# Optimization experiments

Measured on AMD Instinct MI355X. Metric: run time of the kernel, lower is better.

The kernel has to match this reference:

```python
import jax, jax.numpy as jnp
import numpy as np

B, N, DIM, FDIM = 1, 4, 128, 128
H = W = 256          # BEV spatial size
FH = FW = 32         # image feature map size
IMG_H = IMG_W = 256
QW1 = QW2 = 16       # query window
FW1 = FW2 = 2        # feature window
HEADS, DH = 4, 32
LN_EPS = 1e-5
BN_EPS = 1e-5


def _gen_grid(h, w):
    xs = jnp.linspace(0.0, 1.0, w)
    ys = jnp.linspace(0.0, 1.0, h)
    gx, gy = jnp.meshgrid(xs, ys, indexing='xy')
    return jnp.stack([gx, gy, jnp.ones_like(gx)], 0)  # (3, h, w)


def _bev_world():
    # BEVEmbedding.grid0 with bev 256x256, 100m x 100m, offset 0, scale 1
    h_m = w_m = 100.0
    Vm = jnp.array([[0.0, -W / w_m, W / 2.0],
                    [-H / h_m, 0.0, H / 2.0],
                    [0.0, 0.0, 1.0]], dtype=jnp.float32)
    g = _gen_grid(H, W)
    g = g.at[0].multiply(W).at[1].multiply(H)
    g = (jnp.linalg.inv(Vm) @ g.reshape(3, -1)).reshape(3, H, W)
    return g[:2]  # (2, H, W)


def _image_plane():
    p = _gen_grid(FH, FW)
    return p.at[0].multiply(IMG_W).at[1].multiply(IMG_H)  # (3, fh, fw)


def _ln(x, g, b):
    m = x.mean(-1, keepdims=True)
    v = ((x - m) ** 2).mean(-1, keepdims=True)
    return (x - m) * jax.lax.rsqrt(v + LN_EPS) * g + b


def _bn_relu_conv(x, g, b, m, v, w):
    # eval-mode BatchNorm2d -> ReLU -> 1x1 conv (no bias); x: (B*, C, h, w)
    xn = (x - m[:, None, None]) * jax.lax.rsqrt(v[:, None, None] + BN_EPS) * g[:, None, None] + b[:, None, None]
    return jnp.einsum('oi,bihw->bohw', w, jax.nn.relu(xn))


def _part_local(t, w1, w2):
    # 'b n d (x w1) (y w2) -> b n x y w1 w2 d'
    b, n, d, h, w = t.shape
    return t.reshape(b, n, d, h // w1, w1, w // w2, w2).transpose(0, 1, 3, 5, 4, 6, 2)


def _part_grid(t, w1, w2):
    b, n, d, h, w = t.shape
    return t.reshape(b, n, d, w1, h // w1, w2, w // w2).transpose(0, 1, 4, 6, 3, 5, 2)


def _merge(z):
    # 'b x y w1 w2 d -> b (x w1) (y w2) d'
    b, x, y, w1, w2, d = z.shape
    return z.transpose(0, 1, 3, 2, 4, 5).reshape(b, x * w1, y * w2, d)


def _win_attend(q, k, v, nq_g, nq_b, nk_g, nk_b, nv_g, nv_b,
                wq, bq, wk, bk, wv, bv, wp, bp, skip):
    # q: (b,n,X,Y,W1,W2,d); k,v: (b,n,X,Y,F1,F2,d) with X*Y windows matching
    b, n, X, Y, W1, W2, d = q.shape
    F1, F2 = k.shape[4], k.shape[5]
    L = X * Y
    q = q.transpose(0, 2, 3, 1, 4, 5, 6).reshape(b, L, n * W1 * W2, d)
    k = k.transpose(0, 2, 3, 1, 4, 5, 6).reshape(b, L, n * F1 * F2, d)
    v = v.transpose(0, 2, 3, 1, 4, 5, 6).reshape(b, L, n * F1 * F2, d)
    q = (_ln(q, nq_g, nq_b) @ wq.T + bq).reshape(b, L, -1, HEADS, DH)
    k = (_ln(k, nk_g, nk_b) @ wk.T + bk).reshape(b, L, -1, HEADS, DH)
    v = (_ln(v, nv_g, nv_b) @ wv.T + bv).reshape(b, L, -1, HEADS, DH)
    dot = (DH ** -0.5) * jnp.einsum('blqmd,blkmd->blmqk', q, k)
    att = jax.nn.softmax(dot, axis=-1)
    a = jnp.einsum('blmqk,blkmd->blqmd', att, v).reshape(b, L, n * W1 * W2, HEADS * DH)
    z = (a @ wp.T + bp).reshape(b, X, Y, n, W1, W2, d).mean(3)  # mean over views
    return z + skip


def _mlp_res(x, g, b, w1, b1, w2, b2):
    h = _ln(x, g, b)
    h = jax.nn.gelu(h @ w1.T + b1, approximate=False) @ w2.T + b2
    return x + h


def _forward(x, feature, I_inv, E_inv,
             fl_bn_g, fl_bn_b, fl_bn_m, fl_bn_v, fl_w,
             fp_bn_g, fp_bn_b, fp_bn_m, fp_bn_v, fp_w,
             bev_w, bev_b, img_w, cam_w,
             a1_nq_g, a1_nq_b, a1_wq, a1_bq, a1_nk_g, a1_nk_b, a1_wk, a1_bk,
             a1_nv_g, a1_nv_b, a1_wv, a1_bv, a1_wp, a1_bp,
             pn1_g, pn1_b, m1_w1, m1_b1, m1_w2, m1_b2,
             a2_nq_g, a2_nq_b, a2_wq, a2_bq, a2_nk_g, a2_nk_b, a2_wk, a2_bk,
             a2_nv_g, a2_nv_b, a2_wv, a2_bv, a2_wp, a2_bp,
             pn2_g, pn2_b, m2_w1, m2_b1, m2_w2, m2_b2,
             post_g, post_b):
    b, n = feature.shape[:2]
    pixel = _image_plane().reshape(3, -1)                       # (3, fh*fw)
    # camera-center embedding: 1x1 conv (no bias) on E_inv last column
    c_embed = jnp.einsum('oi,bni->bno', cam_w, E_inv[..., -1])  # (b,n,dim)
    # ray directions
    cam = jnp.einsum('bnij,jp->bnip', I_inv, pixel)             # (b,n,3,hw)
    cam = jnp.concatenate([cam, jnp.ones_like(cam[:, :, :1])], 2)
    dvec = jnp.einsum('bnij,bnjp->bnip', E_inv, cam)            # (b,n,4,hw)
    img_embed = jnp.einsum('oi,bnip->bnop', img_w, dvec) - c_embed[..., None]
    img_embed = img_embed / (jnp.linalg.norm(img_embed, axis=2, keepdims=True) + 1e-7)
    img_embed = img_embed.reshape(b, n, DIM, FH, FW)
    # BEV positional embedding
    world = _bev_world()                                        # (2,H,W)
    w_embed = jnp.einsum('oi,ihw->ohw', bev_w, world) + bev_b[:, None, None]
    bev_embed = w_embed[None, None] - c_embed[..., None, None]  # (b,n,dim,H,W)
    query_pos = bev_embed / (jnp.linalg.norm(bev_embed, axis=2, keepdims=True) + 1e-7)
    # key/value features
    feat_flat = feature.reshape(b * n, FDIM, FH, FW)
    key = img_embed + _bn_relu_conv(feat_flat, fp_bn_g, fp_bn_b, fp_bn_m, fp_bn_v, fp_w).reshape(b, n, DIM, FH, FW)
    val = _bn_relu_conv(feat_flat, fl_bn_g, fl_bn_b, fl_bn_m, fl_bn_v, fl_w).reshape(b, n, DIM, FH, FW)
    query = query_pos + x[:, None]                              # (b,n,dim,H,W)
    # stage 1: local window cross-attention
    q1 = _part_local(query, QW1, QW2)
    k1 = _part_local(key, FW1, FW2)
    v1 = _part_local(val, FW1, FW2)
    skip1 = _part_local(x[:, None], QW1, QW2)[:, 0]
    z = _merge(_win_attend(q1, k1, v1, a1_nq_g, a1_nq_b, a1_nk_g, a1_nk_b,
                           a1_nv_g, a1_nv_b, a1_wq, a1_bq, a1_wk, a1_bk,
                           a1_wv, a1_bv, a1_wp, a1_bp, skip1))   # (b,H,W,d)
    z = _mlp_res(z, pn1_g, pn1_b, m1_w1, m1_b1, m1_w2, m1_b2)
    # stage 2: local query windows vs grid-shuffled key/value windows
    q2 = z.reshape(b, H // QW1, QW1, W // QW2, QW2, DIM).transpose(0, 1, 3, 2, 4, 5)
    skip2 = q2
    q2 = jnp.broadcast_to(q2[:, None], (b, n) + q2.shape[1:])
    k2 = _part_grid(key, FW1, FW2)
    v2 = _part_grid(val, FW1, FW2)
    z = _merge(_win_attend(q2, k2, v2, a2_nq_g, a2_nq_b, a2_nk_g, a2_nk_b,
                           a2_nv_g, a2_nv_b, a2_wq, a2_bq, a2_wk, a2_bk,
                           a2_wv, a2_bv, a2_wp, a2_bp, skip2))
    z = _mlp_res(z, pn2_g, pn2_b, m2_w1, m2_b1, m2_w2, m2_b2)
    z = _ln(z, post_g, post_b)
    return z.transpose(0, 3, 1, 2)                              # (b, d, H, W)


def setup_inputs() -> dict:
    ks = iter(jax.random.split(jax.random.key(0), 64))
    rn = lambda *s: jax.random.normal(next(ks), s, jnp.float32)
    w = lambda *s: rn(*s) * 0.05
    d = {'index': 0}
    d['x'] = rn(B, DIM, H, W)
    d['feature'] = rn(B, N, FDIM, FH, FW)
    d['I_inv'] = rn(B, N, 3, 3)
    d['E_inv'] = rn(B, N, 4, 4)
    for p in ('fl', 'fp'):
        d[p + '_bn_g'] = jnp.ones((FDIM,)); d[p + '_bn_b'] = jnp.zeros((FDIM,))
        d[p + '_bn_m'] = jnp.zeros((FDIM,)); d[p + '_bn_v'] = jnp.ones((FDIM,))
        d[p + '_w'] = w(DIM, FDIM)
    d['bev_w'] = w(DIM, 2); d['bev_b'] = jnp.zeros((DIM,))
    d['img_w'] = w(DIM, 4); d['cam_w'] = w(DIM, 4)
    for i in ('1', '2'):
        for t in ('q', 'k', 'v'):
            d['a%s_n%s_g' % (i, t)] = jnp.ones((DIM,))
            d['a%s_n%s_b' % (i, t)] = jnp.zeros((DIM,))
            d['a%s_w%s' % (i, t)] = w(HEADS * DH, DIM)
            d['a%s_b%s' % (i, t)] = jnp.zeros((HEADS * DH,))
        d['a%s_wp' % i] = w(DIM, HEADS * DH); d['a%s_bp' % i] = jnp.zeros((DIM,))
        d['pn%s_g' % i] = jnp.ones((DIM,)); d['pn%s_b' % i] = jnp.zeros((DIM,))
        d['m%s_w1' % i] = w(2 * DIM, DIM); d['m%s_b1' % i] = jnp.zeros((2 * DIM,))
        d['m%s_w2' % i] = w(DIM, 2 * DIM); d['m%s_b2' % i] = jnp.zeros((DIM,))
    d['post_g'] = jnp.ones((DIM,)); d['post_b'] = jnp.zeros((DIM,))
    return d


def reference(index, x, feature, I_inv, E_inv,
              fl_bn_g, fl_bn_b, fl_bn_m, fl_bn_v, fl_w,
              fp_bn_g, fp_bn_b, fp_bn_m, fp_bn_v, fp_w,
              bev_w, bev_b, img_w, cam_w,
              a1_nq_g, a1_nq_b, a1_wq, a1_bq, a1_nk_g, a1_nk_b, a1_wk, a1_bk,
              a1_nv_g, a1_nv_b, a1_wv, a1_bv, a1_wp, a1_bp,
              pn1_g, pn1_b, m1_w1, m1_b1, m1_w2, m1_b2,
              a2_nq_g, a2_nq_b, a2_wq, a2_bq, a2_nk_g, a2_nk_b, a2_wk, a2_bk,
              a2_nv_g, a2_nv_b, a2_wv, a2_bv, a2_wp, a2_bp,
              pn2_g, pn2_b, m2_w1, m2_b1, m2_w2, m2_b2,
              post_g, post_b):
    # index is fixed to 0 (selects bev.grid0, computed internally)
    return _forward(x, feature, I_inv, E_inv,
                    fl_bn_g, fl_bn_b, fl_bn_m, fl_bn_v, fl_w,
                    fp_bn_g, fp_bn_b, fp_bn_m, fp_bn_v, fp_w,
                    bev_w, bev_b, img_w, cam_w,
                    a1_nq_g, a1_nq_b, a1_wq, a1_bq, a1_nk_g, a1_nk_b, a1_wk, a1_bk,
                    a1_nv_g, a1_nv_b, a1_wv, a1_bv, a1_wp, a1_bp,
                    pn1_g, pn1_b, m1_w1, m1_b1, m1_w2, m1_b2,
                    a2_nq_g, a2_nq_b, a2_wq, a2_bq, a2_nk_g, a2_nk_b, a2_wk, a2_bk,
                    a2_nv_g, a2_nv_b, a2_wv, a2_bv, a2_wp, a2_bp,
                    pn2_g, pn2_b, m2_w1, m2_b1, m2_w2, m2_b2,
                    post_g, post_b)
```

## Files before the change

### kernel.cpp

```cpp
#include <hip/hip_runtime.h>
#include <math.h>

#define LN_EPS 1e-5f
#define BN_EPS 1e-5f
#define QK_SCALE 0.1767766953f

typedef __attribute__((ext_vector_type(8))) short bf16x8;
typedef __attribute__((ext_vector_type(4))) float f32x4;

__device__ __forceinline__ unsigned short f2bf(float x) {
    union { float f; unsigned u; } v; v.f = x;
    unsigned r = v.u + 0x7FFFu + ((v.u >> 16) & 1u);
    return (unsigned short)(r >> 16);
}
__device__ __forceinline__ float bf2f(unsigned short h) {
    union { unsigned u; float f; } v; v.u = ((unsigned)h) << 16;
    return v.f;
}
__device__ __forceinline__ unsigned packbf(float a, float b) {
    return (unsigned)f2bf(a) | ((unsigned)f2bf(b) << 16);
}
#define FENCE() asm volatile("" ::: "memory")


__global__ void k_pack(unsigned short* __restrict__ dst, float* __restrict__ cb,
    const float* wq1, const float* wp1, const float* wq2, const float* wp2,
    const float* m1w1, const float* m1w2, const float* m2w1, const float* m2w2,
    const float* fpw, const float* flw,
    const float* wk1, const float* wv1, const float* wk2, const float* wv2,
    const float* bev_b, const float* cam_w, const float* E_inv)
{
    int gid = blockIdx.x * 256 + threadIdx.x;
    if (gid < 294912) {
        const float* src; int off = gid;
        if      (off < 16384)  { src = wq1; }
        else if (off < 32768)  { src = wp1;  off -= 16384; }
        else if (off < 49152)  { src = wq2;  off -= 32768; }
        else if (off < 65536)  { src = wp2;  off -= 49152; }
        else if (off < 98304)  { src = m1w1; off -= 65536; }
        else if (off < 131072) { src = m1w2; off -= 98304; }
        else if (off < 163840) { src = m2w1; off -= 131072; }
        else if (off < 196608) { src = m2w2; off -= 163840; }
        else if (off < 212992) { src = fpw;  off -= 196608; }
        else if (off < 229376) { src = flw;  off -= 212992; }
        else if (off < 245760) { src = wk1;  off -= 229376; }
        else if (off < 262144) { src = wv1;  off -= 245760; }
        else if (off < 278528) { src = wk2;  off -= 262144; }
        else                   { src = wv2;  off -= 278528; }
        dst[gid] = f2bf(src[off]);
    } else if (gid < 311296) {
        int off = gid - 294912;
        dst[gid] = f2bf(wq1[(off & 127)*128 + (off >> 7)]);
    } else if (gid < 327680) {
        int off = gid - 311296;
        dst[gid] = f2bf(wq2[(off & 127)*128 + (off >> 7)]);
    } else if (gid < 328192) {
        int i = gid - 327680;
        int n = i >> 7, c = i & 127;
        const float* Ev = E_inv + n * 16;
        cb[i] = bev_b[c] - (cam_w[c*4+0]*Ev[3] + cam_w[c*4+1]*Ev[7]
                          + cam_w[c*4+2]*Ev[11] + cam_w[c*4+3]*Ev[15]);
    }
}

__global__ void k_img_embed(const float* __restrict__ I_inv,
                            const float* __restrict__ E_inv,
                            const float* __restrict__ img_w,
                            const float* __restrict__ cam_w,
                            float* __restrict__ img_embed)
{
    const int blk = blockIdx.x;
    const int n = blk >> 10, p = blk & 1023;
    const int fy = p >> 5, fx = p & 31;
    const float px = fx * (256.0f / 31.0f);
    const float py = fy * (256.0f / 31.0f);
    const float* Iv = I_inv + n * 9;
    const float* Ev = E_inv + n * 16;
    const float c0 = Iv[0]*px + Iv[1]*py + Iv[2];
    const float c1 = Iv[3]*px + Iv[4]*py + Iv[5];
    const float c2 = Iv[6]*px + Iv[7]*py + Iv[8];
    const float d0 = Ev[0]*c0 + Ev[1]*c1 + Ev[2]*c2 + Ev[3];
    const float d1 = Ev[4]*c0 + Ev[5]*c1 + Ev[6]*c2 + Ev[7];
    const float d2 = Ev[8]*c0 + Ev[9]*c1 + Ev[10]*c2 + Ev[11];
    const float d3 = Ev[12]*c0 + Ev[13]*c1 + Ev[14]*c2 + Ev[15];
    const int c = threadIdx.x;
    const float ce = cam_w[c*4+0]*Ev[3] + cam_w[c*4+1]*Ev[7]
                   + cam_w[c*4+2]*Ev[11] + cam_w[c*4+3]*Ev[15];
    float v = img_w[c*4+0]*d0 + img_w[c*4+1]*d1
            + img_w[c*4+2]*d2 + img_w[c*4+3]*d3 - ce;
    __shared__ float red[128];
    red[c] = v * v;
    __syncthreads();
    for (int s = 64; s > 0; s >>= 1) {
        if (c < s) red[c] += red[c + s];
        __syncthreads();
    }
    img_embed[(n*1024 + p)*128 + c] = v / (sqrtf(red[0]) + 1e-7f);
}

__global__ __launch_bounds__(256) void k_keyval(
    const float* __restrict__ feature,
    const float* __restrict__ img_embed,
    const float* __restrict__ fp_g, const float* __restrict__ fp_b,
    const float* __restrict__ fp_m, const float* __restrict__ fp_v,
    const unsigned short* __restrict__ fpw,
    const float* __restrict__ fl_g, const float* __restrict__ fl_b,
    const float* __restrict__ fl_m, const float* __restrict__ fl_v,
    const unsigned short* __restrict__ flw,
    float* __restrict__ key, float* __restrict__ val)
{
    __shared__ __align__(16) unsigned short aP[64*136];
    __shared__ __align__(16) unsigned short aL[64*136];
    const int n = blockIdx.x >> 4, p0 = (blockIdx.x & 15) * 64;
    const int tid = threadIdx.x;

    for (int idx = tid; idx < 8192; idx += 256) {
        int c = idx >> 6, dt = idx & 63;
        float f = feature[(n*128 + c)*1024 + p0 + dt];
        float xp = (f - fp_m[c]) * rsqrtf(fp_v[c] + BN_EPS) * fp_g[c] + fp_b[c];
        float xl = (f - fl_m[c]) * rsqrtf(fl_v[c] + BN_EPS) * fl_g[c] + fl_b[c];
        aP[dt*136 + c] = f2bf(fmaxf(xp, 0.f));
        aL[dt*136 + c] = f2bf(fmaxf(xl, 0.f));
    }
    __syncthreads();

    const int lane = tid & 63, wid = tid >> 6;
    const int lr = lane & 15, lg = lane >> 4;
    const int wtb = wid * 16;
    f32x4 ak[8], av[8];
    const f32x4 z4 = {0.f, 0.f, 0.f, 0.f};
#pragma unroll
    for (int nf = 0; nf < 8; nf++) { ak[nf] = z4; av[nf] = z4; }
#pragma unroll
    for (int kst = 0; kst < 4; kst++) {
        bf16x8 a1 = *(const bf16x8*)&aP[(wtb+lr)*136 + kst*32 + lg*8];
        bf16x8 a2 = *(const bf16x8*)&aL[(wtb+lr)*136 + kst*32 + lg*8];
#pragma unroll
        for (int nf = 0; nf < 8; nf++) {
            bf16x8 bK = *(const bf16x8*)&fpw[(nf*16+lr)*128 + kst*32 + lg*8];
            bf16x8 bV = *(const bf16x8*)&flw[(nf*16+lr)*128 + kst*32 + lg*8];
            ak[nf] = __builtin_amdgcn_mfma_f32_16x16x32_bf16(a1, bK, ak[nf], 0, 0, 0);
            av[nf] = __builtin_amdgcn_mfma_f32_16x16x32_bf16(a2, bV, av[nf], 0, 0, 0);
        }
    }
#pragma unroll
    for (int nf = 0; nf < 8; nf++) {
#pragma unroll
        for (int rr = 0; rr < 4; rr++) {
            int g = (n*1024 + p0 + wtb + lg*4 + rr)*128 + nf*16 + lr;
            key[g] = ak[nf][rr] + img_embed[g];
            val[g] = av[nf][rr];
        }
    }
}

__global__ __launch_bounds__(256) void k_kvproj(
    const float* __restrict__ key, const float* __restrict__ val,
    const float* __restrict__ k1g, const float* __restrict__ k1b,
    const unsigned short* __restrict__ wk1, const float* __restrict__ bk1,
    const float* __restrict__ v1g, const float* __restrict__ v1b,
    const unsigned short* __restrict__ wv1, const float* __restrict__ bv1,
    const float* __restrict__ k2g, const float* __restrict__ k2b,
    const unsigned short* __restrict__ wk2, const float* __restrict__ bk2,
    const float* __restrict__ v2g, const float* __restrict__ v2b,
    const unsigned short* __restrict__ wv2, const float* __restrict__ bv2,
    float* __restrict__ kp1, float* __restrict__ vp1,
    float* __restrict__ kp2, float* __restrict__ vp2)
{
    __shared__ __align__(16) unsigned short tile[64*136];
    const int pj = blockIdx.x >> 6;
    const int tok0 = (blockIdx.x & 63) * 64;
    const int tid = threadIdx.x;
    const int t = tid >> 2, part = tid & 3;

    const float* gsel[4] = {k1g, v1g, k2g, v2g};
    const float* asel[4] = {k1b, v1b, k2b, v2b};
    const unsigned short* wsel[4] = {wk1, wv1, wk2, wv2};
    const float* bsel[4] = {bk1, bv1, bk2, bv2};
    float* osel[4] = {kp1, vp1, kp2, vp2};
    const float* src = (pj & 1) ? val : key;
    const float* g  = gsel[pj];
    const float* ba = asel[pj];

    float rr_[32];
    float s1 = 0.f, s2 = 0.f;
#pragma unroll
    for (int k4 = 0; k4 < 8; k4++) {
        float4 a = *(const float4*)&src[(tok0+t)*128 + part*32 + k4*4];
        rr_[k4*4+0]=a.x; rr_[k4*4+1]=a.y; rr_[k4*4+2]=a.z; rr_[k4*4+3]=a.w;
        s1 += a.x+a.y+a.z+a.w; s2 += a.x*a.x+a.y*a.y+a.z*a.z+a.w*a.w;
    }
    s1 += __shfl_xor(s1, 1); s1 += __shfl_xor(s1, 2);
    s2 += __shfl_xor(s2, 1); s2 += __shfl_xor(s2, 2);
    const float mean = s1*(1.f/128.f);
    const float var  = s2*(1.f/128.f) - mean*mean;
    const float rstd = rsqrtf(var + LN_EPS);
#pragma unroll
    for (int k = 0; k < 32; k++) {
        int c = part*32 + k;
        float hat = (rr_[k]-mean)*rstd;
        tile[t*136 + c] = f2bf(hat*g[c] + ba[c]);
    }
    FENCE();

    const int lane = tid & 63, wid = tid >> 6;
    const int lr = lane & 15, lg = lane >> 4;
    const int wtb = wid * 16;
    const unsigned short* wp_ = wsel[pj];
    const f32x4 z4 = {0.f, 0.f, 0.f, 0.f};
    f32x4 acc[8];
#pragma unroll
    for (int nf = 0; nf < 8; nf++) acc[nf] = z4;
#pragma unroll
    for (int kst = 0; kst < 4; kst++) {
        bf16x8 a = *(const bf16x8*)&tile[(wtb+lr)*136 + kst*32 + lg*8];
#pragma unroll
        for (int nf = 0; nf < 8; nf++) {
            bf16x8 b = *(const bf16x8*)&wp_[(nf*16+lr)*128 + kst*32 + lg*8];
            acc[nf] = __builtin_amdgcn_mfma_f32_16x16x32_bf16(a, b, acc[nf], 0, 0, 0);
        }
    }
    float* outp = osel[pj];
#pragma unroll
    for (int nf = 0; nf < 8; nf++) {
        float bb = bsel[pj][nf*16 + lr];
#pragma unroll
        for (int rr2 = 0; rr2 < 4; rr2++)
            outp[(tok0 + wtb + lg*4 + rr2)*128 + nf*16 + lr] = acc[nf][rr2] + bb;
    }
}

__global__ __launch_bounds__(256) void k_mwin(
    const float* __restrict__ kp1, const float* __restrict__ kp2,
    const unsigned short* __restrict__ wq1T, const unsigned short* __restrict__ wq2T,
    const float* __restrict__ bq1, const float* __restrict__ bq2,
    unsigned short* __restrict__ Mw1, unsigned short* __restrict__ Mw2,
    float* __restrict__ Mb1, float* __restrict__ Mb2)
{
    __shared__ __align__(16) unsigned short kt[16*136];
    const int blk = blockIdx.x;
    const int stage = blk >> 8, win = blk & 255;
    const int wx = win >> 4, wy = win & 15;
    const int tid = threadIdx.x;

    const float* kp = stage ? kp2 : kp1;
    const unsigned short* wqT = stage ? wq2T : wq1T;
    const float* bq = stage ? bq2 : bq1;
    unsigned short* Mw = stage ? Mw2 : Mw1;
    float* Mb = stage ? Mb2 : Mb1;

    for (int idx = tid; idx < 2048; idx += 256) {
        int c = idx & 127, j = idx >> 7;
        int nk = j >> 2, f1 = (j >> 1) & 1, f2 = j & 1;
        int tok = stage ? (nk*1024 + (f1*16+wx)*32 + (f2*16+wy))
                        : (nk*1024 + (wx*2+f1)*32 + (wy*2+f2));
        kt[j*136 + c] = f2bf(kp[tok*128 + c]);
    }
    __syncthreads();

    const int lane = tid & 63, wid = tid >> 6;
    const int lr = lane & 15, lg = lane >> 4;
    const f32x4 z4 = {0.f, 0.f, 0.f, 0.f};
#pragma unroll
    for (int cc = 0; cc < 2; cc++) {
        int ct = wid*2 + cc;
#pragma unroll
        for (int hd = 0; hd < 4; hd++) {
            bf16x8 a = *(const bf16x8*)&kt[lr*136 + hd*32 + lg*8];
            bf16x8 b = *(const bf16x8*)&wqT[(ct*16+lr)*128 + hd*32 + lg*8];
            f32x4 acc = __builtin_amdgcn_mfma_f32_16x16x32_bf16(a, b, z4, 0, 0, 0);
#pragma unroll
            for (int rr = 0; rr < 4; rr++)
                Mw[((win*4 + hd)*16 + lg*4 + rr)*128 + ct*16 + lr]
                    = f2bf(acc[rr] * QK_SCALE);
        }
    }
    if (tid < 64) {
        int hd = tid >> 4, ky = tid & 15;
        float s = 0.f;
        for (int d = 0; d < 32; d++)
            s += bq[hd*32 + d] * bf2f(kt[ky*136 + hd*32 + d]);
        Mb[win*64 + tid] = s * QK_SCALE;
    }
}

__global__ __launch_bounds__(256) void k_attn1(
    const float* __restrict__ x,
    const float* __restrict__ vp,
    const unsigned short* __restrict__ mw, const float* __restrict__ mb,
    const float* __restrict__ bev_w, const float* __restrict__ cb,
    const float* __restrict__ nqg, const float* __restrict__ nqb,
    const unsigned short* __restrict__ wpp, const float* __restrict__ bp,
    float* __restrict__ z1)
{
    __shared__ __align__(16) unsigned short aT[64*136];
    __shared__ __align__(16) unsigned short mws[64*136];
    __shared__ __align__(16) unsigned short vbT[128*24];
    __shared__ __align__(16) unsigned short xbuf[64*132];
    __shared__ float mbs[64];
    __shared__ float cbs[512];
    __shared__ float nqgs[128];
    __shared__ float nqbs[128];

    const int blk = blockIdx.x;
    const int win = blk >> 2, rg = blk & 3;
    const int wx = win >> 4, wy = win & 15;
    const int tid = threadIdx.x;
    const int lane = tid & 63, wid = tid >> 6;
    const int lr = lane & 15, lg = lane >> 4;
    const int wtb = wid * 16;

    for (int idx = tid; idx < 2048; idx += 256) {
        int c = idx & 127, j = idx >> 7;
        int nk = j >> 2, f1 = (j >> 1) & 1, f2 = j & 1;
        int src = (nk*1024 + (wx*2+f1)*32 + (wy*2+f2))*128 + c;
        vbT[c*24 + j] = f2bf(vp[src]);
    }
    {
        const unsigned short* mwsrc = mw + win*8192;
        for (int idx = tid; idx < 2048; idx += 256) {
            int row = idx >> 5, c4 = (idx & 31)*4;
            *(ushort4*)&mws[row*136 + c4] = *(const ushort4*)&mwsrc[row*128 + c4];
        }
    }
    for (int idx = tid; idx < 8192; idx += 256) {
        int tt = idx & 63, c = idx >> 6;
        int hh = wx*16 + rg*4 + (tt >> 4), ww = wy*16 + (tt & 15);
        xbuf[tt*132 + c] = f2bf(x[c*65536 + hh*256 + ww]);
    }
    if (tid < 64) mbs[tid] = mb[win*64 + tid];
    for (int idx = tid; idx < 512; idx += 256) cbs[idx] = cb[idx];
    if (tid < 128) { nqgs[tid] = nqg[tid]; nqbs[tid] = nqb[tid]; }

    const int t = tid >> 2, part = tid & 3;
    const int w1 = rg*4 + (t >> 4), w2 = t & 15;
    const int h = wx*16 + w1, w = wy*16 + w2;
    const float world0 = 50.f - (float)h * (100.f/255.f);
    const float world1 = 50.f - (float)w * (100.f/255.f);

    float xv[32];
#pragma unroll
    for (int k = 0; k < 32; k++) xv[k] = x[(part*32+k)*65536 + h*256 + w];
    float base_[32];
#pragma unroll
    for (int k = 0; k < 32; k++) {
        int c = part*32 + k;
        base_[k] = bev_w[c*2+0]*world0 + bev_w[c*2+1]*world1;
    }
    __syncthreads();

    f32x4 aacc[4][2];
    const f32x4 z4 = {0.f, 0.f, 0.f, 0.f};
#pragma unroll
    for (int hd = 0; hd < 4; hd++) { aacc[hd][0] = z4; aacc[hd][1] = z4; }

    uint2 pa[4], pb[4];

    auto do_view = [&](int n, uint2* pp) {
        float r[32]; float ss = 0.f;
#pragma unroll
        for (int k = 0; k < 32; k++) {
            int c = part*32 + k;
            float e = base_[k] + cbs[n*128 + c];
            r[k] = e; ss += e*e;
        }
        ss += __shfl_xor(ss, 1); ss += __shfl_xor(ss, 2);
        const float invn = 1.f / (sqrtf(ss) + 1e-7f);
        float s1 = 0.f, s2 = 0.f;
#pragma unroll
        for (int k = 0; k < 32; k++) {
            float qv = r[k]*invn + xv[k];
            r[k] = qv; s1 += qv; s2 += qv*qv;
        }
        s1 += __shfl_xor(s1, 1); s1 += __shfl_xor(s1, 2);
        s2 += __shfl_xor(s2, 1); s2 += __shfl_xor(s2, 2);
        const float mean = s1*(1.f/128.f);
        const float var  = s2*(1.f/128.f) - mean*mean;
        const float rstd = rsqrtf(var + LN_EPS);
#pragma unroll
        for (int k4 = 0; k4 < 8; k4++) {
            int c = part*32 + k4*4;
            ushort4 u;
            u.x = f2bf((r[k4*4+0]-mean)*rstd*nqgs[c+0] + nqbs[c+0]);
            u.y = f2bf((r[k4*4+1]-mean)*rstd*nqgs[c+1] + nqbs[c+1]);
            u.z = f2bf((r[k4*4+2]-mean)*rstd*nqgs[c+2] + nqbs[c+2]);
            u.w = f2bf((r[k4*4+3]-mean)*rstd*nqgs[c+3] + nqbs[c+3]);
            *(ushort4*)&aT[t*136 + c] = u;
        }
        FENCE();

        f32x4 sacc[4];
#pragma unroll
        for (int hd = 0; hd < 4; hd++) sacc[hd] = z4;
#pragma unroll
        for (int kst = 0; kst < 4; kst++) {
            bf16x8 bq_ = *(const bf16x8*)&aT[(wtb+lr)*136 + kst*32 + lg*8];
#pragma unroll
            for (int hd = 0; hd < 4; hd++) {
                bf16x8 am = *(const bf16x8*)&mws[(hd*16 + lr)*136 + kst*32 + lg*8];
                sacc[hd] = __builtin_amdgcn_mfma_f32_16x16x32_bf16(am, bq_, sacc[hd], 0, 0, 0);
            }
        }
#pragma unroll
        for (int hd = 0; hd < 4; hd++) {
            float e0 = sacc[hd][0] + mbs[hd*16 + lg*4 + 0];
            float e1 = sacc[hd][1] + mbs[hd*16 + lg*4 + 1];
            float e2 = sacc[hd][2] + mbs[hd*16 + lg*4 + 2];
            float e3 = sacc[hd][3] + mbs[hd*16 + lg*4 + 3];
            float mx = fmaxf(fmaxf(e0, e1), fmaxf(e2, e3));
            mx = fmaxf(mx, __shfl_xor(mx, 16));
            mx = fmaxf(mx, __shfl_xor(mx, 32));
            e0 = __expf(e0-mx); e1 = __expf(e1-mx);
            e2 = __expf(e2-mx); e3 = __expf(e3-mx);
            float sum = e0+e1+e2+e3;
            sum += __shfl_xor(sum, 16);
            sum += __shfl_xor(sum, 32);
            float is = 1.f/sum;
            pp[hd] = make_uint2(packbf(e0*is, e1*is), packbf(e2*is, e3*is));
        }
        FENCE();
    };

    auto pv_pair = [&]() {
        const int s0 = (lg & 1)*32 + lr;
        const int s1 = s0 + 16;
        const bool hi = (lg >> 1) != 0;
#pragma unroll
        for (int hd = 0; hd < 4; hd++) {
            unsigned a00 = __shfl(pa[hd].x, s0), a01 = __shfl(pa[hd].y, s0);
            unsigned a10 = __shfl(pa[hd].x, s1), a11 = __shfl(pa[hd].y, s1);
            unsigned b00 = __shfl(pb[hd].x, s0), b01 = __shfl(pb[hd].y, s0);
            unsigned b10 = __shfl(pb[hd].x, s1), b11 = __shfl(pb[hd].y, s1);
            union { unsigned u[4]; bf16x8 v; } af;
            af.u[0] = hi ? b00 : a00; af.u[1] = hi ? b01 : a01;
            af.u[2] = hi ? b10 : a10; af.u[3] = hi ? b11 : a11;
#pragma unroll
            for (int dt = 0; dt < 2; dt++) {
                bf16x8 bv = *(const bf16x8*)&vbT[(hd*32+dt*16+lr)*24 + (lg&1)*8];
                aacc[hd][dt] = __builtin_amdgcn_mfma_f32_16x16x32_bf16(af.v, bv, aacc[hd][dt], 0, 0, 0);
            }
        }
    };

    do_view(0, pa); do_view(1, pb); pv_pair();
    do_view(2, pa); do_view(3, pb); pv_pair();

#pragma unroll
    for (int hd = 0; hd < 4; hd++)
#pragma unroll
        for (int dt = 0; dt < 2; dt++)
#pragma unroll
            for (int rr = 0; rr < 4; rr++)
                aT[(wtb + lg*4 + rr)*136 + hd*32 + dt*16 + lr]
                    = f2bf(aacc[hd][dt][rr] * 0.25f);
    FENCE();

    f32x4 acc[8];
#pragma unroll
    for (int nf = 0; nf < 8; nf++) acc[nf] = z4;
#pragma unroll
    for (int kst = 0; kst < 4; kst++) {
        bf16x8 a = *(const bf16x8*)&aT[(wtb+lr)*136 + kst*32 + lg*8];
#pragma unroll
        for (int nf = 0; nf < 8; nf++) {
            bf16x8 b = *(const bf16x8*)&wpp[(nf*16+lr)*128 + kst*32 + lg*8];
            acc[nf] = __builtin_amdgcn_mfma_f32_16x16x32_bf16(a, b, acc[nf], 0, 0, 0);
        }
    }
#pragma unroll
    for (int nf = 0; nf < 8; nf++) {
        float bpv = bp[nf*16 + lr];
#pragma unroll
        for (int rr = 0; rr < 4; rr++) {
            int tt = wtb + lg*4 + rr;
            int hh = wx*16 + rg*4 + (tt >> 4), ww = wy*16 + (tt & 15);
            float res = bf2f(xbuf[tt*132 + nf*16 + lr]);
            z1[(hh*256+ww)*128 + nf*16 + lr] = acc[nf][rr] + bpv + res;
        }
    }
}

__global__ __launch_bounds__(256) void k_attn2(
    const float* __restrict__ z1,
    const float* __restrict__ vp,
    const unsigned short* __restrict__ mw, const float* __restrict__ mb,
    const float* __restrict__ nqg, const float* __restrict__ nqb,
    const unsigned short* __restrict__ wpp, const float* __restrict__ bp,
    float* __restrict__ z2)
{
    __shared__ __align__(16) unsigned short aT[64*136];
    __shared__ __align__(16) unsigned short vbT[128*24];
    __shared__ float mbs[64];

    const int blk = blockIdx.x;
    const int win = blk >> 2, rg = blk & 3;
    const int wx = win >> 4, wy = win & 15;
    const int tid = threadIdx.x;
    const int lane = tid & 63, wid = tid >> 6;
    const int lr = lane & 15, lg = lane >> 4;
    const int wtb = wid * 16;

    for (int idx = tid; idx < 2048; idx += 256) {
        int c = idx & 127, j = idx >> 7;
        int nk = j >> 2, f1 = (j >> 1) & 1, f2 = j & 1;
        int src = (nk*1024 + (f1*16+wx)*32 + (f2*16+wy))*128 + c;
        vbT[c*24 + j] = f2bf(vp[src]);
    }
    if (tid < 64) mbs[tid] = mb[win*64 + tid];

    const int t = tid >> 2, part = tid & 3;
    const int w1 = rg*4 + (t >> 4), w2 = t & 15;
    const int h = wx*16 + w1, w = wy*16 + w2;
    const float* zr = z1 + (h*256 + w)*128 + part*32;

    float r[32]; float s1 = 0.f, s2 = 0.f;
#pragma unroll
    for (int k4 = 0; k4 < 8; k4++) {
        float4 v = *(const float4*)&zr[k4*4];
        r[k4*4+0]=v.x; r[k4*4+1]=v.y; r[k4*4+2]=v.z; r[k4*4+3]=v.w;
        s1 += v.x+v.y+v.z+v.w;
        s2 += v.x*v.x+v.y*v.y+v.z*v.z+v.w*v.w;
    }
    s1 += __shfl_xor(s1, 1); s1 += __shfl_xor(s1, 2);
    s2 += __shfl_xor(s2, 1); s2 += __shfl_xor(s2, 2);
    const float mean = s1*(1.f/128.f);
    const float var  = s2*(1.f/128.f) - mean*mean;
    const float rstd = rsqrtf(var + LN_EPS);
#pragma unroll
    for (int k4 = 0; k4 < 8; k4++) {
        int c = part*32 + k4*4;
        ushort4 u;
        u.x = f2bf((r[k4*4+0]-mean)*rstd*nqg[c+0] + nqb[c+0]);
        u.y = f2bf((r[k4*4+1]-mean)*rstd*nqg[c+1] + nqb[c+1]);
        u.z = f2bf((r[k4*4+2]-mean)*rstd*nqg[c+2] + nqb[c+2]);
        u.w = f2bf((r[k4*4+3]-mean)*rstd*nqg[c+3] + nqb[c+3]);
        *(ushort4*)&aT[t*136 + c] = u;
    }
    __syncthreads();

    const f32x4 z4 = {0.f, 0.f, 0.f, 0.f};
    f32x4 sacc[4];
#pragma unroll
    for (int hd = 0; hd < 4; hd++) sacc[hd] = z4;
#pragma unroll
    for (int kst = 0; kst < 4; kst++) {
        bf16x8 bq_ = *(const bf16x8*)&aT[(wtb+lr)*136 + kst*32 + lg*8];
#pragma unroll
        for (int hd = 0; hd < 4; hd++) {
            bf16x8 am = *(const bf16x8*)&mw[((win*4+hd)*16 + lr)*128 + kst*32 + lg*8];
            sacc[hd] = __builtin_amdgcn_mfma_f32_16x16x32_bf16(am, bq_, sacc[hd], 0, 0, 0);
        }
    }
    uint2 pa[4];
#pragma unroll
    for (int hd = 0; hd < 4; hd++) {
        float e0 = sacc[hd][0] + mbs[hd*16 + lg*4 + 0];
        float e1 = sacc[hd][1] + mbs[hd*16 + lg*4 + 1];
        float e2 = sacc[hd][2] + mbs[hd*16 + lg*4 + 2];
        float e3 = sacc[hd][3] + mbs[hd*16 + lg*4 + 3];
        float mx = fmaxf(fmaxf(e0, e1), fmaxf(e2, e3));
        mx = fmaxf(mx, __shfl_xor(mx, 16));
        mx = fmaxf(mx, __shfl_xor(mx, 32));
        e0 = __expf(e0-mx); e1 = __expf(e1-mx);
        e2 = __expf(e2-mx); e3 = __expf(e3-mx);
        float sum = e0+e1+e2+e3;
        sum += __shfl_xor(sum, 16);
        sum += __shfl_xor(sum, 32);
        float is = 1.f/sum;
        pa[hd] = make_uint2(packbf(e0*is, e1*is), packbf(e2*is, e3*is));
    }

    f32x4 aacc[4][2];
#pragma unroll
    for (int hd = 0; hd < 4; hd++) { aacc[hd][0] = z4; aacc[hd][1] = z4; }
    {
        const int s0 = (lg & 1)*32 + lr;
        const int s1_ = s0 + 16;
        const bool hi = (lg >> 1) != 0;
#pragma unroll
        for (int hd = 0; hd < 4; hd++) {
            unsigned a00 = __shfl(pa[hd].x, s0), a01 = __shfl(pa[hd].y, s0);
            unsigned a10 = __shfl(pa[hd].x, s1_), a11 = __shfl(pa[hd].y, s1_);
            union { unsigned u[4]; bf16x8 v; } af;
            af.u[0] = hi ? 0u : a00; af.u[1] = hi ? 0u : a01;
            af.u[2] = hi ? 0u : a10; af.u[3] = hi ? 0u : a11;
#pragma unroll
            for (int dt = 0; dt < 2; dt++) {
                bf16x8 bv = *(const bf16x8*)&vbT[(hd*32+dt*16+lr)*24 + (lg&1)*8];
                aacc[hd][dt] = __builtin_amdgcn_mfma_f32_16x16x32_bf16(af.v, bv, aacc[hd][dt], 0, 0, 0);
            }
        }
    }
    FENCE();
#pragma unroll
    for (int hd = 0; hd < 4; hd++)
#pragma unroll
        for (int dt = 0; dt < 2; dt++)
#pragma unroll
            for (int rr = 0; rr < 4; rr++)
                aT[(wtb + lg*4 + rr)*136 + hd*32 + dt*16 + lr]
                    = f2bf(aacc[hd][dt][rr]);
    FENCE();

    f32x4 acc[8];
#pragma unroll
    for (int nf = 0; nf < 8; nf++) acc[nf] = z4;
#pragma unroll
    for (int kst = 0; kst < 4; kst++) {
        bf16x8 a = *(const bf16x8*)&aT[(wtb+lr)*136 + kst*32 + lg*8];
#pragma unroll
        for (int nf = 0; nf < 8; nf++) {
            bf16x8 b = *(const bf16x8*)&wpp[(nf*16+lr)*128 + kst*32 + lg*8];
            acc[nf] = __builtin_amdgcn_mfma_f32_16x16x32_bf16(a, b, acc[nf], 0, 0, 0);
        }
    }
#pragma unroll
    for (int nf = 0; nf < 8; nf++) {
        float bpv = bp[nf*16 + lr];
#pragma unroll
        for (int rr = 0; rr < 4; rr++) {
            int tt = wtb + lg*4 + rr;
            int hh = wx*16 + rg*4 + (tt >> 4), ww = wy*16 + (tt & 15);
            int gi = (hh*256+ww)*128 + nf*16 + lr;
            z2[gi] = acc[nf][rr] + bpv + z1[gi];
        }
    }
}

__global__ __launch_bounds__(256) void k_mlp(
    float* __restrict__ z,
    const float* __restrict__ g, const float* __restrict__ bta,
    const unsigned short* __restrict__ w1p, const float* __restrict__ b1,
    const unsigned short* __restrict__ w2p, const float* __restrict__ b2)
{
    __shared__ __align__(16) unsigned short aT[64*136];
    __shared__ __align__(16) unsigned short hT[64*136];
    const int base = blockIdx.x * 64;
    const int tid = threadIdx.x;
    const int t = tid >> 2, part = tid & 3;

    const float* zr = z + (base + t)*128 + part*32;
    float r[32]; float s1 = 0.f, s2 = 0.f;
#pragma unroll
    for (int k4 = 0; k4 < 8; k4++) {
        float4 v = *(const float4*)&zr[k4*4];
        r[k4*4+0]=v.x; r[k4*4+1]=v.y; r[k4*4+2]=v.z; r[k4*4+3]=v.w;
        s1 += v.x+v.y+v.z+v.w;
        s2 += v.x*v.x+v.y*v.y+v.z*v.z+v.w*v.w;
    }
    s1 += __shfl_xor(s1, 1); s1 += __shfl_xor(s1, 2);
    s2 += __shfl_xor(s2, 1); s2 += __shfl_xor(s2, 2);
    const float mean = s1*(1.f/128.f);
    const float var  = s2*(1.f/128.f) - mean*mean;
    const float rstd = rsqrtf(var + LN_EPS);
#pragma unroll
    for (int k4 = 0; k4 < 8; k4++) {
        int c = part*32 + k4*4;
        ushort4 u;
        u.x = f2bf((r[k4*4+0]-mean)*rstd*g[c+0] + bta[c+0]);
        u.y = f2bf((r[k4*4+1]-mean)*rstd*g[c+1] + bta[c+1]);
        u.z = f2bf((r[k4*4+2]-mean)*rstd*g[c+2] + bta[c+2]);
        u.w = f2bf((r[k4*4+3]-mean)*rstd*g[c+3] + bta[c+3]);
        *(ushort4*)&aT[t*136 + c] = u;
    }
    __syncthreads();

    const int lane = tid & 63, wid = tid >> 6;
    const int lr = lane & 15, lg = lane >> 4;
    const int wtb = wid * 16;
    const f32x4 z4 = {0.f, 0.f, 0.f, 0.f};

    f32x4 oacc[8];
#pragma unroll
    for (int nf = 0; nf < 8; nf++) oacc[nf] = z4;

#pragma unroll
    for (int half = 0; half < 2; half++) {
        f32x4 acc[8];
#pragma unroll
        for (int nf = 0; nf < 8; nf++) acc[nf] = z4;
#pragma unroll
        for (int kst = 0; kst < 4; kst++) {
            bf16x8 a = *(const bf16x8*)&aT[(wtb+lr)*136 + kst*32 + lg*8];
#pragma unroll
            for (int nf = 0; nf < 8; nf++) {
                bf16x8 b = *(const bf16x8*)&w1p[((half*8+nf)*16+lr)*128 + kst*32 + lg*8];
                acc[nf] = __builtin_amdgcn_mfma_f32_16x16x32_bf16(a, b, acc[nf], 0, 0, 0);
            }
        }
#pragma unroll
        for (int nf = 0; nf < 8; nf++) {
            float bb = b1[(half*8+nf)*16 + lr];
#pragma unroll
            for (int rr = 0; rr < 4; rr++) {
                float hv = acc[nf][rr] + bb;
                float gl = 0.5f*hv*(1.f + erff(hv*0.70710678118f));
                hT[(wtb + lg*4 + rr)*136 + nf*16 + lr] = f2bf(gl);
            }
        }
        FENCE();

#pragma unroll
        for (int kst = 0; kst < 4; kst++) {
            bf16x8 a = *(const bf16x8*)&hT[(wtb+lr)*136 + kst*32 + lg*8];
#pragma unroll
            for (int nf = 0; nf < 8; nf++) {
                bf16x8 b = *(const bf16x8*)&w2p[(nf*16+lr)*256 + half*128 + kst*32 + lg*8];
                oacc[nf] = __builtin_amdgcn_mfma_f32_16x16x32_bf16(a, b, oacc[nf], 0, 0, 0);
            }
        }
        FENCE();
    }

#pragma unroll
    for (int nf = 0; nf < 8; nf++) {
        float bb = b2[nf*16 + lr];
#pragma unroll
        for (int rr = 0; rr < 4; rr++) {
            int idx = (base + wtb + lg*4 + rr)*128 + nf*16 + lr;
            z[idx] = z[idx] + oacc[nf][rr] + bb;
        }
    }
}

__global__ __launch_bounds__(256) void k_post(
    const float* __restrict__ z2,
    const float* __restrict__ g, const float* __restrict__ b,
    float* __restrict__ out)
{
    __shared__ float buf[64][129];
    const int blk = blockIdx.x;
    const int h = blk >> 2, w0 = (blk & 3)*64;
    const int tid = threadIdx.x;
    const int t = tid >> 2, part = tid & 3;

    const float* zr = z2 + (h*256 + w0 + t)*128 + part*32;
    float r[32]; float s1 = 0.f, s2 = 0.f;
#pragma unroll
    for (int k4 = 0; k4 < 8; k4++) {
        float4 v = *(const float4*)&zr[k4*4];
        r[k4*4+0]=v.x; r[k4*4+1]=v.y; r[k4*4+2]=v.z; r[k4*4+3]=v.w;
        s1 += v.x+v.y+v.z+v.w;
        s2 += v.x*v.x+v.y*v.y+v.z*v.z+v.w*v.w;
    }
    s1 += __shfl_xor(s1, 1); s1 += __shfl_xor(s1, 2);
    s2 += __shfl_xor(s2, 1); s2 += __shfl_xor(s2, 2);
    const float mean = s1*(1.f/128.f);
    const float var  = s2*(1.f/128.f) - mean*mean;
    const float rstd = rsqrtf(var + LN_EPS);
#pragma unroll
    for (int k = 0; k < 32; k++) {
        int c = part*32 + k;
        buf[t][c] = (r[k]-mean)*rstd*g[c] + b[c];
    }
    __syncthreads();
    for (int idx = tid; idx < 64*128; idx += 256) {
        int c = idx >> 6, wl = idx & 63;
        out[(c*256 + h)*256 + w0 + wl] = buf[wl][c];
    }
}

extern "C" void kernel_launch(void* const* d_in, const int* in_sizes, int n_in,
                              void* d_out, int out_size, void* d_ws, size_t ws_size,
                              hipStream_t stream)
{
    (void)in_sizes; (void)n_in; (void)out_size; (void)ws_size;
    const float* x       = (const float*)d_in[1];
    const float* feature = (const float*)d_in[2];
    const float* I_inv   = (const float*)d_in[3];
    const float* E_inv   = (const float*)d_in[4];
    const float* fl_g = (const float*)d_in[5],  *fl_b = (const float*)d_in[6];
    const float* fl_m = (const float*)d_in[7],  *fl_v = (const float*)d_in[8];
    const float* fl_w = (const float*)d_in[9];
    const float* fp_g = (const float*)d_in[10], *fp_b = (const float*)d_in[11];
    const float* fp_m = (const float*)d_in[12], *fp_v = (const float*)d_in[13];
    const float* fp_w = (const float*)d_in[14];
    const float* bev_w = (const float*)d_in[15], *bev_b = (const float*)d_in[16];
    const float* img_w = (const float*)d_in[17], *cam_w = (const float*)d_in[18];
    const float* a1_nq_g = (const float*)d_in[19], *a1_nq_b = (const float*)d_in[20];
    const float* a1_wq = (const float*)d_in[21], *a1_bq = (const float*)d_in[22];
    const float* a1_nk_g = (const float*)d_in[23], *a1_nk_b = (const float*)d_in[24];
    const float* a1_wk = (const float*)d_in[25], *a1_bk = (const float*)d_in[26];
    const float* a1_nv_g = (const float*)d_in[27], *a1_nv_b = (const float*)d_in[28];
    const float* a1_wv = (const float*)d_in[29], *a1_bv = (const float*)d_in[30];
    const float* a1_wp = (const float*)d_in[31], *a1_bp = (const float*)d_in[32];
    const float* pn1_g = (const float*)d_in[33], *pn1_b = (const float*)d_in[34];
    const float* m1_w1 = (const float*)d_in[35], *m1_b1 = (const float*)d_in[36];
    const float* m1_w2 = (const float*)d_in[37], *m1_b2 = (const float*)d_in[38];
    const float* a2_nq_g = (const float*)d_in[39], *a2_nq_b = (const float*)d_in[40];
    const float* a2_wq = (const float*)d_in[41], *a2_bq = (const float*)d_in[42];
    const float* a2_nk_g = (const float*)d_in[43], *a2_nk_b = (const float*)d_in[44];
    const float* a2_wk = (const float*)d_in[45], *a2_bk = (const float*)d_in[46];
    const float* a2_nv_g = (const float*)d_in[47], *a2_nv_b = (const float*)d_in[48];
    const float* a2_wv = (const float*)d_in[49], *a2_bv = (const float*)d_in[50];
    const float* a2_wp = (const float*)d_in[51], *a2_bp = (const float*)d_in[52];
    const float* pn2_g = (const float*)d_in[53], *pn2_b = (const float*)d_in[54];
    const float* m2_w1 = (const float*)d_in[55], *m2_b1 = (const float*)d_in[56];
    const float* m2_w2 = (const float*)d_in[57], *m2_b2 = (const float*)d_in[58];
    const float* post_g = (const float*)d_in[59], *post_b = (const float*)d_in[60];

    float* ws  = (float*)d_ws;
    unsigned short* pk = (unsigned short*)ws;
    const unsigned short* wp1p  = pk + 16384;
    const unsigned short* wp2p  = pk + 49152;
    const unsigned short* m1w1p = pk + 65536;
    const unsigned short* m1w2p = pk + 98304;
    const unsigned short* m2w1p = pk + 131072;
    const unsigned short* m2w2p = pk + 163840;
    const unsigned short* fpwp  = pk + 196608;
    const unsigned short* flwp  = pk + 212992;
    const unsigned short* wk1p  = pk + 229376;
    const unsigned short* wv1p  = pk + 245760;
    const unsigned short* wk2p  = pk + 262144;
    const unsigned short* wv2p  = pk + 278528;
    const unsigned short* wq1Tp = pk + 294912;
    const unsigned short* wq2Tp = pk + 311296;

    float* cb  = ws + 163840;
    float* Mb1 = ws + 164352;
    float* Mb2 = ws + 180736;
    float* kp2 = ws + 197120;
    float* vp2 = ws + 721408;
    unsigned short* Mw2 = (unsigned short*)(ws + 1245696);
    float* kp1 = ws + 2294272;
    float* vp1 = ws + 2818560;
    unsigned short* Mw1 = (unsigned short*)(ws + 3342848);
    float* key = ws + 3342848;
    float* val = ws + 3867136;
    float* img = ws + 4391424;
    float* z2  = ws + 2294272;
    float* z1  = (float*)d_out;

    k_pack<<<1283, 256, 0, stream>>>(pk, cb,
        a1_wq, a1_wp, a2_wq, a2_wp, m1_w1, m1_w2, m2_w1, m2_w2,
        fp_w, fl_w, a1_wk, a1_wv, a2_wk, a2_wv, bev_b, cam_w, E_inv);
    k_img_embed<<<4096, 128, 0, stream>>>(I_inv, E_inv, img_w, cam_w, img);
    k_keyval<<<64, 256, 0, stream>>>(feature, img,
                                     fp_g, fp_b, fp_m, fp_v, fpwp,
                                     fl_g, fl_b, fl_m, fl_v, flwp,
                                     key, val);
    k_kvproj<<<256, 256, 0, stream>>>(key, val,
                                      a1_nk_g, a1_nk_b, wk1p, a1_bk,
                                      a1_nv_g, a1_nv_b, wv1p, a1_bv,
                                      a2_nk_g, a2_nk_b, wk2p, a2_bk,
                                      a2_nv_g, a2_nv_b, wv2p, a2_bv,
                                      kp1, vp1, kp2, vp2);
    k_mwin<<<512, 256, 0, stream>>>(kp1, kp2, wq1Tp, wq2Tp, a1_bq, a2_bq,
                                    Mw1, Mw2, Mb1, Mb2);
    k_attn1<<<1024, 256, 0, stream>>>(x, vp1, Mw1, Mb1, bev_w, cb,
                                      a1_nq_g, a1_nq_b, wp1p, a1_bp, z1);
    k_mlp<<<1024, 256, 0, stream>>>(z1, pn1_g, pn1_b, m1w1p, m1_b1, m1w2p, m1_b2);
    k_attn2<<<1024, 256, 0, stream>>>(z1, vp2, Mw2, Mb2,
                                      a2_nq_g, a2_nq_b, wp2p, a2_bp, z2);
    k_mlp<<<1024, 256, 0, stream>>>(z2, pn2_g, pn2_b, m2w1p, m2_b1, m2w2p, m2_b2);
    k_post<<<1024, 256, 0, stream>>>(z2, post_g, post_b, (float*)d_out);
}
```

Before: 391.5 us.

## Process 128 rows per MLP block to reuse weight fragments across two row tiles

The MLP kernel now handles 128 tokens per block instead of 64, so each wave computes two 16-row tiles and every weight fragment loaded from global memory feeds two MFMAs. The hidden dimension is processed in four 64-wide chunks, which shrinks the shared hidden buffer, and the grid is halved. The aim is to halve weight load traffic per token. The cost is more accumulator registers, fewer blocks to fill the CUs, and a larger shared-memory footprint.

```diff
diff --git a/kernel.cpp b/kernel.cpp
--- a/kernel.cpp
+++ b/kernel.cpp
@@ -633,35 +633,38 @@
     const unsigned short* __restrict__ w1p, const float* __restrict__ b1,
     const unsigned short* __restrict__ w2p, const float* __restrict__ b2)
 {
-    __shared__ __align__(16) unsigned short aT[64*136];
-    __shared__ __align__(16) unsigned short hT[64*136];
-    const int base = blockIdx.x * 64;
+    __shared__ __align__(16) unsigned short aT[128*136];
+    __shared__ __align__(16) unsigned short hT[128*72];
+    const int base = blockIdx.x * 128;
     const int tid = threadIdx.x;
     const int t = tid >> 2, part = tid & 3;
 
-    const float* zr = z + (base + t)*128 + part*32;
-    float r[32]; float s1 = 0.f, s2 = 0.f;
-#pragma unroll
-    for (int k4 = 0; k4 < 8; k4++) {
-        float4 v = *(const float4*)&zr[k4*4];
-        r[k4*4+0]=v.x; r[k4*4+1]=v.y; r[k4*4+2]=v.z; r[k4*4+3]=v.w;
-        s1 += v.x+v.y+v.z+v.w;
-        s2 += v.x*v.x+v.y*v.y+v.z*v.z+v.w*v.w;
-    }
-    s1 += __shfl_xor(s1, 1); s1 += __shfl_xor(s1, 2);
-    s2 += __shfl_xor(s2, 1); s2 += __shfl_xor(s2, 2);
-    const float mean = s1*(1.f/128.f);
-    const float var  = s2*(1.f/128.f) - mean*mean;
-    const float rstd = rsqrtf(var + LN_EPS);
-#pragma unroll
-    for (int k4 = 0; k4 < 8; k4++) {
-        int c = part*32 + k4*4;
-        ushort4 u;
-        u.x = f2bf((r[k4*4+0]-mean)*rstd*g[c+0] + bta[c+0]);
-        u.y = f2bf((r[k4*4+1]-mean)*rstd*g[c+1] + bta[c+1]);
-        u.z = f2bf((r[k4*4+2]-mean)*rstd*g[c+2] + bta[c+2]);
-        u.w = f2bf((r[k4*4+3]-mean)*rstd*g[c+3] + bta[c+3]);
-        *(ushort4*)&aT[t*136 + c] = u;
+#pragma unroll
+    for (int rt = 0; rt < 2; rt++) {
+        const float* zr = z + (base + rt*64 + t)*128 + part*32;
+        float r[32]; float s1 = 0.f, s2 = 0.f;
+#pragma unroll
+        for (int k4 = 0; k4 < 8; k4++) {
+            float4 v = *(const float4*)&zr[k4*4];
+            r[k4*4+0]=v.x; r[k4*4+1]=v.y; r[k4*4+2]=v.z; r[k4*4+3]=v.w;
+            s1 += v.x+v.y+v.z+v.w;
+            s2 += v.x*v.x+v.y*v.y+v.z*v.z+v.w*v.w;
+        }
+        s1 += __shfl_xor(s1, 1); s1 += __shfl_xor(s1, 2);
+        s2 += __shfl_xor(s2, 1); s2 += __shfl_xor(s2, 2);
+        const float mean = s1*(1.f/128.f);
+        const float var  = s2*(1.f/128.f) - mean*mean;
+        const float rstd = rsqrtf(var + LN_EPS);
+#pragma unroll
+        for (int k4 = 0; k4 < 8; k4++) {
+            int c = part*32 + k4*4;
+            ushort4 u;
+            u.x = f2bf((r[k4*4+0]-mean)*rstd*g[c+0] + bta[c+0]);
+            u.y = f2bf((r[k4*4+1]-mean)*rstd*g[c+1] + bta[c+1]);
+            u.z = f2bf((r[k4*4+2]-mean)*rstd*g[c+2] + bta[c+2]);
+            u.w = f2bf((r[k4*4+3]-mean)*rstd*g[c+3] + bta[c+3]);
+            *(ushort4*)&aT[(rt*64 + t)*136 + c] = u;
+        }
     }
     __syncthreads();
 
@@ -670,43 +673,53 @@
     const int wtb = wid * 16;
     const f32x4 z4 = {0.f, 0.f, 0.f, 0.f};
 
-    f32x4 oacc[8];
-#pragma unroll
-    for (int nf = 0; nf < 8; nf++) oacc[nf] = z4;
-
-#pragma unroll
-    for (int half = 0; half < 2; half++) {
-        f32x4 acc[8];
-#pragma unroll
-        for (int nf = 0; nf < 8; nf++) acc[nf] = z4;
+    f32x4 oacc[2][8];
+#pragma unroll
+    for (int rt = 0; rt < 2; rt++)
+#pragma unroll
+        for (int nf = 0; nf < 8; nf++) oacc[rt][nf] = z4;
+
+#pragma unroll
+    for (int q = 0; q < 4; q++) {
+        f32x4 acc[2][4];
+#pragma unroll
+        for (int rt = 0; rt < 2; rt++)
+#pragma unroll
+            for (int nf = 0; nf < 4; nf++) acc[rt][nf] = z4;
 #pragma unroll
         for (int kst = 0; kst < 4; kst++) {
-            bf16x8 a = *(const bf16x8*)&aT[(wtb+lr)*136 + kst*32 + lg*8];
+            bf16x8 a0 = *(const bf16x8*)&aT[(wtb+lr)*136 + kst*32 + lg*8];
+            bf16x8 a1 = *(const bf16x8*)&aT[(64+wtb+lr)*136 + kst*32 + lg*8];
+#pragma unroll
+            for (int nf = 0; nf < 4; nf++) {
+                bf16x8 b = *(const bf16x8*)&w1p[((q*4+nf)*16+lr)*128 + kst*32 + lg*8];
+                acc[0][nf] = __builtin_amdgcn_mfma_f32_16x16x32_bf16(a0, b, acc[0][nf], 0, 0, 0);
+                acc[1][nf] = __builtin_amdgcn_mfma_f32_16x16x32_bf16(a1, b, acc[1][nf], 0, 0, 0);
+            }
+        }
+#pragma unroll
+        for (int nf = 0; nf < 4; nf++) {
+            float bb = b1[(q*4+nf)*16 + lr];
+#pragma unroll
+            for (int rt = 0; rt < 2; rt++)
+#pragma unroll
+                for (int rr = 0; rr < 4; rr++) {
+                    float hv = acc[rt][nf][rr] + bb;
+                    float gl = 0.5f*hv*(1.f + erff(hv*0.70710678118f));
+                    hT[(rt*64 + wtb + lg*4 + rr)*72 + nf*16 + lr] = f2bf(gl);
+                }
+        }
+        FENCE();
+
+#pragma unroll
+        for (int kst2 = 0; kst2 < 2; kst2++) {
+            bf16x8 a0 = *(const bf16x8*)&hT[(wtb+lr)*72 + kst2*32 + lg*8];
+            bf16x8 a1 = *(const bf16x8*)&hT[(64+wtb+lr)*72 + kst2*32 + lg*8];
 #pragma unroll
             for (int nf = 0; nf < 8; nf++) {
-                bf16x8 b = *(const bf16x8*)&w1p[((half*8+nf)*16+lr)*128 + kst*32 + lg*8];
-                acc[nf] = __builtin_amdgcn_mfma_f32_16x16x32_bf16(a, b, acc[nf], 0, 0, 0);
-            }
-        }
-#pragma unroll
-        for (int nf = 0; nf < 8; nf++) {
-            float bb = b1[(half*8+nf)*16 + lr];
-#pragma unroll
-            for (int rr = 0; rr < 4; rr++) {
-                float hv = acc[nf][rr] + bb;
-                float gl = 0.5f*hv*(1.f + erff(hv*0.70710678118f));
-                hT[(wtb + lg*4 + rr)*136 + nf*16 + lr] = f2bf(gl);
-            }
-        }
-        FENCE();
-
-#pragma unroll
-        for (int kst = 0; kst < 4; kst++) {
-            bf16x8 a = *(const bf16x8*)&hT[(wtb+lr)*136 + kst*32 + lg*8];
-#pragma unroll
-            for (int nf = 0; nf < 8; nf++) {
-                bf16x8 b = *(const bf16x8*)&w2p[(nf*16+lr)*256 + half*128 + kst*32 + lg*8];
-                oacc[nf] = __builtin_amdgcn_mfma_f32_16x16x32_bf16(a, b, oacc[nf], 0, 0, 0);
+                bf16x8 b = *(const bf16x8*)&w2p[(nf*16+lr)*256 + q*64 + kst2*32 + lg*8];
+                oacc[0][nf] = __builtin_amdgcn_mfma_f32_16x16x32_bf16(a0, b, oacc[0][nf], 0, 0, 0);
+                oacc[1][nf] = __builtin_amdgcn_mfma_f32_16x16x32_bf16(a1, b, oacc[1][nf], 0, 0, 0);
             }
         }
         FENCE();
@@ -716,10 +729,12 @@
     for (int nf = 0; nf < 8; nf++) {
         float bb = b2[nf*16 + lr];
 #pragma unroll
-        for (int rr = 0; rr < 4; rr++) {
-            int idx = (base + wtb + lg*4 + rr)*128 + nf*16 + lr;
-            z[idx] = z[idx] + oacc[nf][rr] + bb;
-        }
+        for (int rt = 0; rt < 2; rt++)
+#pragma unroll
+            for (int rr = 0; rr < 4; rr++) {
+                int idx = (base + rt*64 + wtb + lg*4 + rr)*128 + nf*16 + lr;
+                z[idx] = z[idx] + oacc[rt][nf][rr] + bb;
+            }
     }
 }
 
@@ -849,9 +864,9 @@
                                     Mw1, Mw2, Mb1, Mb2);
     k_attn1<<<1024, 256, 0, stream>>>(x, vp1, Mw1, Mb1, bev_w, cb,
                                       a1_nq_g, a1_nq_b, wp1p, a1_bp, z1);
-    k_mlp<<<1024, 256, 0, stream>>>(z1, pn1_g, pn1_b, m1w1p, m1_b1, m1w2p, m1_b2);
+    k_mlp<<<512, 256, 0, stream>>>(z1, pn1_g, pn1_b, m1w1p, m1_b1, m1w2p, m1_b2);
     k_attn2<<<1024, 256, 0, stream>>>(z1, vp2, Mw2, Mb2,
                                       a2_nq_g, a2_nq_b, wp2p, a2_bp, z2);
-    k_mlp<<<1024, 256, 0, stream>>>(z2, pn2_g, pn2_b, m2w1p, m2_b1, m2w2p, m2_b2);
+    k_mlp<<<512, 256, 0, stream>>>(z2, pn2_g, pn2_b, m2w1p, m2_b1, m2w2p, m2_b2);
     k_post<<<1024, 256, 0, stream>>>(z2, post_g, post_b, (float*)d_out);
 }
```

Result: slower. 442.0 us (+12.9%).
